# Performance work log

Hardware: AMD Instinct MI355X
Metric: run time of the kernel (lower is better)

## Reference

```python
import jax, jax.numpy as jnp
import numpy as np

B, S, D = 8, 2048, 512  # batch, seq_len, d_model (= units*heads = 64*8)


def setup_inputs() -> dict:
    key = jax.random.key(0)
    k1, k2, k3, k4 = jax.random.split(key, 4)
    scale = 1.0 / np.sqrt(D)
    return {
        "data": jax.random.normal(k1, (B, S, D), dtype=jnp.float32),
        "Wq": jax.random.normal(k2, (D, D), dtype=jnp.float32) * scale,
        "Wk": jax.random.normal(k3, (D, D), dtype=jnp.float32) * scale,
        "Wv": jax.random.normal(k4, (D, D), dtype=jnp.float32) * scale,
    }


def reference(data, Wq, Wk, Wv):
    # Bias-free projections (no head split in the original module).
    q = data @ Wq  # [B,S,D]
    k = data @ Wk
    v = data @ Wv
    scores = jnp.einsum("bsd,btd->bst", q, k)  # [B,S,S]
    # NOTE: original scales by sqrt(weight.shape[-1]) == sqrt(seq_len), not sqrt(d_k).
    scores = scores / jnp.sqrt(jnp.float32(scores.shape[-1]))
    # Causal mask: (w + 1e6) * tril - 1e6  ==  where(tril, w, -1e6)
    causal = jnp.tril(jnp.ones((scores.shape[1], scores.shape[2]), dtype=bool))
    scores = jnp.where(causal[None, :, :], scores, jnp.float32(-1e6))
    attn = jax.nn.softmax(scores, axis=-1)
    return jnp.einsum("bst,btd->bsd", attn, v)  # [B,S,D]
```

## Files before the change

### kernel.cpp

```cpp
#include <hip/hip_runtime.h>

typedef unsigned short u16;
typedef __attribute__((ext_vector_type(8))) short short8;
typedef __attribute__((ext_vector_type(4))) float f32x4;


__device__ __forceinline__ u16 f2bf(float f) {
    unsigned u = __float_as_uint(f);
    u += 0x7fffu + ((u >> 16) & 1u);
    return (u16)(u >> 16);
}

__device__ __forceinline__ void lds_cp16(const u16* g, u16* l) {
#if defined(__has_builtin) && __has_builtin(__builtin_amdgcn_global_load_lds)
    __builtin_amdgcn_global_load_lds(
        (const __attribute__((address_space(1))) void*)g,
        (__attribute__((address_space(3))) void*)l, 16, 0, 0);
#else
    *(uint4*)l = *(const uint4*)g;
#endif
}

template <int MI, bool ROWSUM>
__device__ __forceinline__ void gemm64(const u16* __restrict__ Ag, int lda,
                                       const u16* __restrict__ Bg, int ldb,
                                       int ksteps, u16* Alds, u16* Blds,
                                       f32x4 (&acc)[MI][4], f32x4* accL) {
    const int t = threadIdx.x;
    const int lane = t & 63, w = t >> 6;
    const int l15 = lane & 15, g4 = lane >> 4;
    const int wr = (w >> 1) * (MI * 16);
    const int wc = (w & 1) * 64;
    const int swz = l15 & 7;
    const short ob = (short)0x3f80;
    const short8 ones = {ob, ob, ob, ob, ob, ob, ob, ob};

    for (int kt = 0; kt < ksteps; ++kt) {
        __syncthreads();
#pragma unroll
        for (int p = 0; p < MI; ++p) {
            const int gi = t + p * 256;
            const int row = gi >> 3;
            const int gl = (gi & 7) ^ (row & 7);
            lds_cp16(Ag + (size_t)row * lda + kt * 64 + gl * 8, Alds + gi * 8);
        }
#pragma unroll
        for (int p = 0; p < 4; ++p) {
            const int gi = t + p * 256;
            const int row = gi >> 3;
            const int gl = (gi & 7) ^ (row & 7);
            lds_cp16(Bg + (size_t)row * ldb + kt * 64 + gl * 8, Blds + gi * 8);
        }
        __syncthreads();
#pragma unroll
        for (int ks = 0; ks < 2; ++ks) {
            short8 a[MI], b[4];
#pragma unroll
            for (int i = 0; i < MI; ++i) {
                const int r = wr + i * 16 + l15;
                a[i] = *(const short8*)(Alds + r * 64 + (((ks * 4 + g4) ^ swz) * 8));
            }
#pragma unroll
            for (int j = 0; j < 4; ++j) {
                const int r = wc + j * 16 + l15;
                b[j] = *(const short8*)(Blds + r * 64 + (((ks * 4 + g4) ^ swz) * 8));
            }
#pragma unroll
            for (int i = 0; i < MI; ++i)
#pragma unroll
                for (int j = 0; j < 4; ++j)
                    acc[i][j] = __builtin_amdgcn_mfma_f32_16x16x32_bf16(a[i], b[j], acc[i][j], 0, 0, 0);
            if constexpr (ROWSUM) {
#pragma unroll
                for (int i = 0; i < MI; ++i)
                    accL[i] = __builtin_amdgcn_mfma_f32_16x16x32_bf16(a[i], ones, accL[i], 0, 0, 0);
            }
        }
    }
}


__global__ void k_cvt_x(const float4* __restrict__ X, ushort4* __restrict__ Xb, int n4) {
    for (int i = blockIdx.x * blockDim.x + threadIdx.x; i < n4; i += gridDim.x * blockDim.x) {
        float4 v = X[i];
        ushort4 o;
        o.x = f2bf(v.x); o.y = f2bf(v.y); o.z = f2bf(v.z); o.w = f2bf(v.w);
        Xb[i] = o;
    }
}

__global__ void k_cvt_w(const float* __restrict__ Wq, const float* __restrict__ Wk,
                        const float* __restrict__ Wv, u16* __restrict__ Wt) {
    int idx = blockIdx.x * 256 + threadIdx.x;
    int z = idx >> 18;
    int rem = idx & 262143;
    float v;
    if (z == 0) v = Wq[rem];
    else if (z == 1) v = Wk[rem];
    else { int n = rem >> 9, k = rem & 511; v = Wv[k * 512 + n]; }
    Wt[idx] = f2bf(v);
}

__global__ __launch_bounds__(256, 4) void k_gemm_m(const u16* __restrict__ Wt, u16* __restrict__ Mt) {
    __shared__ alignas(16) u16 Alds[8192];
    __shared__ alignas(16) u16 Blds[8192];
    const int mt = blockIdx.x & 3, nt = blockIdx.x >> 2;
    const u16* Ag = Wt + 0 * 512 * 512 + (size_t)mt * 128 * 512;
    const u16* Bg = Wt + 1 * 512 * 512 + (size_t)nt * 128 * 512;
    f32x4 acc[4][4] = {};
    gemm64<4, false>(Ag, 512, Bg, 512, 8, Alds, Blds, acc, (f32x4*)nullptr);

    const int t = threadIdx.x, lane = t & 63, w = t >> 6;
    const int wr = (w >> 1) * 64, wc = (w & 1) * 64;
    const float sc = 0.022097086912079608f;
#pragma unroll
    for (int i = 0; i < 4; ++i)
#pragma unroll
        for (int j = 0; j < 4; ++j)
#pragma unroll
            for (int r = 0; r < 4; ++r) {
                int e = mt * 128 + wr + i * 16 + 4 * (lane >> 4) + r;
                int f = nt * 128 + wc + j * 16 + (lane & 15);
                Mt[(size_t)f * 512 + e] = f2bf(acc[i][j][r] * sc);
            }
}

__global__ __launch_bounds__(256, 4) void k_proj(const u16* __restrict__ Xb, const u16* __restrict__ Wt,
                                                 const u16* __restrict__ Mt,
                                                 u16* __restrict__ Gb, u16* __restrict__ Vt) {
    __shared__ alignas(16) u16 Alds[8192];
    __shared__ alignas(16) u16 Blds[8192];
    const int bid = blockIdx.x;
    const int u = bid >> 3;
    const int z = u >> 6;
    const int nt = (u >> 4) & 3;
    const int mt = (bid & 7) * 16 + (u & 15);
    const u16* Ag = Xb + (size_t)mt * 128 * 512;
    const u16* Bg = (z == 0) ? (Mt + (size_t)nt * 128 * 512)
                             : (Wt + 2 * 512 * 512 + (size_t)nt * 128 * 512);
    f32x4 acc[4][4] = {};
    gemm64<4, false>(Ag, 512, Bg, 512, 8, Alds, Blds, acc, (f32x4*)nullptr);

    const int t = threadIdx.x, lane = t & 63, w = t >> 6;
    const int wr = (w >> 1) * 64, wc = (w & 1) * 64;
    if (z == 0) {
#pragma unroll
        for (int i = 0; i < 4; ++i)
#pragma unroll
            for (int j = 0; j < 4; ++j)
#pragma unroll
                for (int r = 0; r < 4; ++r) {
                    int m = mt * 128 + wr + i * 16 + 4 * (lane >> 4) + r;
                    int n = nt * 128 + wc + j * 16 + (lane & 15);
                    Gb[(size_t)m * 512 + n] = f2bf(acc[i][j][r]);
                }
    } else {
        int b = mt >> 4;
#pragma unroll
        for (int i = 0; i < 4; ++i)
#pragma unroll
            for (int j = 0; j < 4; ++j) {
                int s0 = (mt * 128 + wr + i * 16 + 4 * (lane >> 4)) & 2047;
                int d = nt * 128 + wc + j * 16 + (lane & 15);
                ushort4 pk;
                pk.x = f2bf(acc[i][j][0]); pk.y = f2bf(acc[i][j][1]);
                pk.z = f2bf(acc[i][j][2]); pk.w = f2bf(acc[i][j][3]);
                *(ushort4*)(Vt + (size_t)b * 512 * 2048 + (size_t)d * 2048 + s0) = pk;
            }
    }
}

__global__ __launch_bounds__(256, 4) void k_scores(const u16* __restrict__ Gb, const u16* __restrict__ Xb,
                                                   u16* __restrict__ P) {
    const int bid = blockIdx.x;
    const int bz = bid & 7;
    const int tt = bid >> 3;
    int qi = (int)((sqrtf(8.0f * tt + 1.0f) - 1.0f) * 0.5f);
    while ((qi + 1) * (qi + 2) / 2 <= tt) ++qi;
    while (qi * (qi + 1) / 2 > tt) --qi;
    const int kvj = tt - qi * (qi + 1) / 2;

    __shared__ alignas(16) u16 Alds[8192];
    __shared__ alignas(16) u16 Blds[8192];
    const u16* Ag = Gb + (size_t)bz * 2048 * 512 + (size_t)qi * 128 * 512;
    const u16* Bg = Xb + (size_t)bz * 2048 * 512 + (size_t)kvj * 128 * 512;
    f32x4 acc[4][4] = {};
    gemm64<4, false>(Ag, 512, Bg, 512, 8, Alds, Blds, acc, (f32x4*)nullptr);

    const int t = threadIdx.x, lane = t & 63, w = t >> 6;
    const int wr = (w >> 1) * 64, wc = (w & 1) * 64;
    u16* Pb = P + (size_t)bz * 2048 * 2048;
#pragma unroll
    for (int i = 0; i < 4; ++i)
#pragma unroll
        for (int j = 0; j < 4; ++j)
#pragma unroll
            for (int r = 0; r < 4; ++r) {
                int q = qi * 128 + wr + i * 16 + 4 * (lane >> 4) + r;
                int kv = kvj * 128 + wc + j * 16 + (lane & 15);
                float pv = (kv <= q) ? __expf(acc[i][j][r]) : 0.0f;
                Pb[(size_t)q * 2048 + kv] = f2bf(pv);
            }
}

__global__ __launch_bounds__(256, 4) void k_pv(const u16* __restrict__ P, const u16* __restrict__ Vt,
                                               float* __restrict__ Out) {
    __shared__ alignas(16) u16 Alds[4096];
    __shared__ alignas(16) u16 Blds[8192];
    const int bid = blockIdx.x;
    const int bz = bid & 7;
    const int u = bid >> 3;
    const int g = u >> 5;
    const int s = u & 31;
    const int nt = g;
    const int qi2 = (g & 1) ? (31 - s) : s;
    const int ksteps = qi2 + 1;

    const u16* Ag = P + (size_t)bz * 2048 * 2048 + (size_t)qi2 * 64 * 2048;
    const u16* Bg = Vt + (size_t)bz * 512 * 2048 + (size_t)nt * 128 * 2048;
    f32x4 acc[2][4] = {};
    f32x4 accL[2] = {};
    gemm64<2, true>(Ag, 2048, Bg, 2048, ksteps, Alds, Blds, acc, accL);

    const int t = threadIdx.x, lane = t & 63, w = t >> 6;
    const int l = lane & 15, g4 = lane >> 4;
    const int wr = (w >> 1) * 32, wc = (w & 1) * 64;
#pragma unroll
    for (int i = 0; i < 2; ++i) {
        float inv[4];
#pragma unroll
        for (int r = 0; r < 4; ++r) inv[r] = 1.0f / accL[i][r];
#pragma unroll
        for (int j = 0; j < 4; ++j) {
            const int d = nt * 128 + wc + j * 16 + l;
#pragma unroll
            for (int r = 0; r < 4; ++r) {
                const int q = qi2 * 64 + wr + i * 16 + 4 * g4 + r;
                Out[(size_t)bz * 2048 * 512 + (size_t)q * 512 + d] = acc[i][j][r] * inv[r];
            }
        }
    }
}


extern "C" void kernel_launch(void* const* d_in, const int* in_sizes, int n_in,
                              void* d_out, int out_size, void* d_ws, size_t ws_size,
                              hipStream_t stream) {
    const float* data = (const float*)d_in[0];
    const float* Wq = (const float*)d_in[1];
    const float* Wk = (const float*)d_in[2];
    const float* Wv = (const float*)d_in[3];
    float* out = (float*)d_out;
    char* ws = (char*)d_ws;

    u16* Xb = (u16*)(ws);
    u16* Gb = (u16*)(ws + 16777216);
    u16* Mt = (u16*)(ws + 33554432);
    u16* Vt = (u16*)(ws + 50331648);
    u16* Wt = (u16*)(ws + 67108864);
    u16* P  = (u16*)(ws + 68681728);

    k_cvt_x<<<2048, 256, 0, stream>>>((const float4*)data, (ushort4*)Xb, (8 * 2048 * 512) / 4);
    k_cvt_w<<<3072, 256, 0, stream>>>(Wq, Wk, Wv, Wt);
    k_gemm_m<<<16, 256, 0, stream>>>(Wt, Mt);
    k_proj<<<1024, 256, 0, stream>>>(Xb, Wt, Mt, Gb, Vt);
    k_scores<<<1088, 256, 0, stream>>>(Gb, Xb, P);
    k_pv<<<1024, 256, 0, stream>>>(P, Vt, out);
}
```

Measured before the change: 112.4 us.

## Merge conversion kernels and stagger GEMM block start with s_sleep skew

Combines the activation and weight bf16 conversion kernels into one launch, with each weight-path thread converting four elements, to save a kernel launch. It also adds a per-block startup delay, proportional to block index in groups of 256, before the GEMM main loop in the projection, scores and PV kernels. The delay is meant to stagger waves so that memory bursts and LDS contention spread out. In exchange, later blocks sit idle before starting, which adds latency.

```diff
diff --git a/kernel.cpp b/kernel.cpp
--- a/kernel.cpp
+++ b/kernel.cpp
@@ -19,6 +19,11 @@
 #else
     *(uint4*)l = *(const uint4*)g;
 #endif
+}
+
+__device__ __forceinline__ void skew(int bid) {
+    const int slot = bid >> 8;
+    for (int i = 0; i < slot; ++i) __builtin_amdgcn_s_sleep(7);
 }
 
 template <int MI, bool ROWSUM>
@@ -80,25 +85,32 @@
 }
 
 
-__global__ void k_cvt_x(const float4* __restrict__ X, ushort4* __restrict__ Xb, int n4) {
-    for (int i = blockIdx.x * blockDim.x + threadIdx.x; i < n4; i += gridDim.x * blockDim.x) {
-        float4 v = X[i];
-        ushort4 o;
-        o.x = f2bf(v.x); o.y = f2bf(v.y); o.z = f2bf(v.z); o.w = f2bf(v.w);
-        Xb[i] = o;
-    }
-}
-
-__global__ void k_cvt_w(const float* __restrict__ Wq, const float* __restrict__ Wk,
-                        const float* __restrict__ Wv, u16* __restrict__ Wt) {
-    int idx = blockIdx.x * 256 + threadIdx.x;
-    int z = idx >> 18;
-    int rem = idx & 262143;
-    float v;
-    if (z == 0) v = Wq[rem];
-    else if (z == 1) v = Wk[rem];
-    else { int n = rem >> 9, k = rem & 511; v = Wv[k * 512 + n]; }
-    Wt[idx] = f2bf(v);
+__global__ void k_cvt(const float4* __restrict__ X4, ushort4* __restrict__ Xb4,
+                      const float* __restrict__ Wq, const float* __restrict__ Wk,
+                      const float* __restrict__ Wv, u16* __restrict__ Wt) {
+    const int bid = blockIdx.x, t = threadIdx.x;
+    if (bid < 2048) {
+        const int n4 = (8 * 2048 * 512) / 4;
+        for (int i = bid * 256 + t; i < n4; i += 2048 * 256) {
+            float4 v = X4[i];
+            ushort4 o;
+            o.x = f2bf(v.x); o.y = f2bf(v.y); o.z = f2bf(v.z); o.w = f2bf(v.w);
+            Xb4[i] = o;
+        }
+    } else {
+        const int e0 = ((bid - 2048) * 256 + t) * 4;
+#pragma unroll
+        for (int p = 0; p < 4; ++p) {
+            const int idx = e0 + p;
+            const int z = idx >> 18;
+            const int rem = idx & 262143;
+            float v;
+            if (z == 0) v = Wq[rem];
+            else if (z == 1) v = Wk[rem];
+            else { int n = rem >> 9, k = rem & 511; v = Wv[k * 512 + n]; }
+            Wt[idx] = f2bf(v);
+        }
+    }
 }
 
 __global__ __launch_bounds__(256, 4) void k_gemm_m(const u16* __restrict__ Wt, u16* __restrict__ Mt) {
@@ -138,6 +150,7 @@
     const u16* Ag = Xb + (size_t)mt * 128 * 512;
     const u16* Bg = (z == 0) ? (Mt + (size_t)nt * 128 * 512)
                              : (Wt + 2 * 512 * 512 + (size_t)nt * 128 * 512);
+    skew(bid);
     f32x4 acc[4][4] = {};
     gemm64<4, false>(Ag, 512, Bg, 512, 8, Alds, Blds, acc, (f32x4*)nullptr);
 
@@ -184,6 +197,7 @@
     __shared__ alignas(16) u16 Blds[8192];
     const u16* Ag = Gb + (size_t)bz * 2048 * 512 + (size_t)qi * 128 * 512;
     const u16* Bg = Xb + (size_t)bz * 2048 * 512 + (size_t)kvj * 128 * 512;
+    skew(bid);
     f32x4 acc[4][4] = {};
     gemm64<4, false>(Ag, 512, Bg, 512, 8, Alds, Blds, acc, (f32x4*)nullptr);
 
@@ -218,6 +232,7 @@
 
     const u16* Ag = P + (size_t)bz * 2048 * 2048 + (size_t)qi2 * 64 * 2048;
     const u16* Bg = Vt + (size_t)bz * 512 * 2048 + (size_t)nt * 128 * 2048;
+    skew(bid);
     f32x4 acc[2][4] = {};
     f32x4 accL[2] = {};
     gemm64<2, true>(Ag, 2048, Bg, 2048, ksteps, Alds, Blds, acc, accL);
@@ -260,8 +275,7 @@
     u16* Wt = (u16*)(ws + 67108864);
     u16* P  = (u16*)(ws + 68681728);
 
-    k_cvt_x<<<2048, 256, 0, stream>>>((const float4*)data, (ushort4*)Xb, (8 * 2048 * 512) / 4);
-    k_cvt_w<<<3072, 256, 0, stream>>>(Wq, Wk, Wv, Wt);
+    k_cvt<<<2816, 256, 0, stream>>>((const float4*)data, (ushort4*)Xb, Wq, Wk, Wv, Wt);
     k_gemm_m<<<16, 256, 0, stream>>>(Wt, Mt);
     k_proj<<<1024, 256, 0, stream>>>(Xb, Wt, Mt, Gb, Vt);
     k_scores<<<1088, 256, 0, stream>>>(Gb, Xb, P);
```

Measured after the change: 111.0 us. No clear change (-1.3%).
